# Optimization experiments

Hardware: AMD Instinct MI355X
Metric: run time of the kernel (lower is better)

The kernel has to match this reference:

```python
import jax, jax.numpy as jnp
import numpy as np

B, T, DIM = 2, 2048, 1024
H, HKV, D = 16, 4, 64
ROPE_DIMS = 32
ROPE_BASE = 10000.0


def fake_quant(w, n_bits):
    # per-output-row absmax symmetric fake quantization with STE
    half = 2 ** (n_bits - 1)
    w_max = jnp.maximum(jnp.max(jnp.abs(w), axis=1, keepdims=True), 1e-5)
    w_int = jnp.clip(jnp.round(w / w_max * half), -half, half - 1)
    w_q = w_int / half * w_max
    return w + jax.lax.stop_gradient(w_q - w)


def rms_norm(x):
    eps = jnp.finfo(x.dtype).eps
    return x * jax.lax.rsqrt(jnp.mean(x * x, axis=-1, keepdims=True) + eps)


def rope_tables(seq_len, dtype):
    inv_freq = 1.0 / (ROPE_BASE ** (jnp.arange(0, ROPE_DIMS, 2, dtype=jnp.float32) / ROPE_DIMS))
    t = jnp.arange(seq_len, dtype=jnp.float32)
    freqs = t[:, None] * inv_freq[None, :]  # [T, rope_dims/2]
    return jnp.cos(freqs).astype(dtype)[None, None], jnp.sin(freqs).astype(dtype)[None, None]


def apply_rotary(x, cos, sin):
    # partial rotary: rotate first ROPE_DIMS dims, pass the rest through
    x_rope, x_pass = x[..., :ROPE_DIMS], x[..., ROPE_DIMS:]
    half = ROPE_DIMS // 2
    x1, x2 = x_rope[..., :half], x_rope[..., half:]
    rot = jnp.concatenate([x1 * cos + x2 * sin, -x1 * sin + x2 * cos], axis=-1)
    return jnp.concatenate([rot, x_pass], axis=-1)


def setup_inputs() -> dict:
    key = jax.random.key(0)
    ks = jax.random.split(key, 5)
    kv_dim = HKV * D
    return {
        "x": jax.random.normal(ks[0], (B, T, DIM), dtype=jnp.float32),
        "w_q": jax.random.normal(ks[1], (DIM, DIM), dtype=jnp.float32) * 0.02,
        "w_k": jax.random.normal(ks[2], (kv_dim, DIM), dtype=jnp.float32) * 0.02,
        "w_v": jax.random.normal(ks[3], (kv_dim, DIM), dtype=jnp.float32) * 0.02,
        "w_proj": jax.random.normal(ks[4], (DIM, DIM), dtype=jnp.float32) * 0.02,
        "q_gain": jnp.full((H,), 1.5, dtype=jnp.float32),
    }


def reference(x, w_q, w_k, w_v, w_proj, q_gain):
    bsz, seqlen, dim = x.shape
    group = H // HKV

    # quantized (STE) projections
    q = x @ fake_quant(w_q, 6).T        # [B, T, DIM]
    k = x @ fake_quant(w_k, 6).T        # [B, T, HKV*D]
    v = x @ fake_quant(w_v, 5).T        # [B, T, HKV*D]

    q = q.reshape(bsz, seqlen, H, D).transpose(0, 2, 1, 3)    # [B, H, T, D]
    k = k.reshape(bsz, seqlen, HKV, D).transpose(0, 2, 1, 3)  # [B, HKV, T, D]
    v = v.reshape(bsz, seqlen, HKV, D).transpose(0, 2, 1, 3)  # [B, HKV, T, D]

    q = rms_norm(q)
    k = rms_norm(k)

    cos, sin = rope_tables(seqlen, q.dtype)
    q = apply_rotary(q, cos, sin)
    k = apply_rotary(k, cos, sin)

    q = q * q_gain.astype(q.dtype)[None, :, None, None]

    # grouped-query causal attention; scores kept in grouped [B,HKV,g,T,T] layout
    qg = q.reshape(bsz, HKV, group, seqlen, D)
    scores = jnp.einsum('bhgqd,bhkd->bhgqk', qg, k) / jnp.sqrt(jnp.asarray(D, q.dtype))
    causal = jnp.tril(jnp.ones((seqlen, seqlen), dtype=bool))
    scores = jnp.where(causal[None, None, None], scores, jnp.asarray(-jnp.inf, scores.dtype))
    att = jax.nn.softmax(scores, axis=-1)
    y = jnp.einsum('bhgqk,bhkd->bhgqd', att, v)               # [B, HKV, g, T, D]

    # xsa: orthogonalize y against normalized v (per kv head group)
    y_g = y.transpose(0, 3, 1, 2, 4)                           # [B, T, HKV, g, D]
    v_t = v.transpose(0, 2, 1, 3)                              # [B, T, HKV, D]
    vn = v_t / jnp.maximum(jnp.linalg.norm(v_t, axis=-1, keepdims=True), 1e-12)
    vn = vn[..., None, :]                                      # [B, T, HKV, 1, D]
    proj = jnp.sum(y_g * vn, axis=-1, keepdims=True) * vn
    y_out = (y_g - proj).reshape(bsz, seqlen, dim)

    return y_out @ fake_quant(w_proj, 5).T
```

## Files before the change

### kernel.cpp

```cpp
#include <hip/hip_runtime.h>
#include <math.h>

typedef unsigned short u16;
typedef __attribute__((ext_vector_type(8))) short short8;
typedef __attribute__((ext_vector_type(4))) float float4v;
typedef __attribute__((ext_vector_type(4))) u16 ushort4v;

namespace {
constexpr int kT    = 2048;
constexpr int kDim  = 1024;
constexpr int kH    = 16;
constexpr int kHKV  = 4;
constexpr int kD    = 64;
constexpr int kTok  = 4096;
constexpr int kQKVN = 1536;
}

__device__ __forceinline__ u16 f2bf(float f) {
  unsigned int u = __builtin_bit_cast(unsigned int, f);
  u = (u + 0x7FFFu + ((u >> 16) & 1u)) >> 16;
  return (u16)u;
}

__global__ __launch_bounds__(256) void prep_kernel(
    const float* __restrict__ x,
    const float* __restrict__ w_q, const float* __restrict__ w_k,
    const float* __restrict__ w_v, const float* __restrict__ w_proj,
    u16* __restrict__ xb, u16* __restrict__ wqkv, u16* __restrict__ wpq,
    float2* __restrict__ ropetab)
{
  __shared__ float red[4];
  const int bid = blockIdx.x, tid = threadIdx.x;

  if (bid < 128) {
    const int idx = bid * 256 + tid;
    const int t = idx >> 4, i = idx & 15;
    const float fr = (float)t * powf(10000.0f, -(float)i * (1.0f / 16.0f));
    ropetab[idx] = make_float2(cosf(fr), sinf(fr));
    return;
  }
  if (bid < 2176) {
    const size_t i = ((size_t)(bid - 128) * 256 + tid) * 8;
    const float4 a = *(const float4*)(x + i);
    const float4 b = *(const float4*)(x + i + 4);
    short8 r;
    r[0] = (short)f2bf(a.x); r[1] = (short)f2bf(a.y);
    r[2] = (short)f2bf(a.z); r[3] = (short)f2bf(a.w);
    r[4] = (short)f2bf(b.x); r[5] = (short)f2bf(b.y);
    r[6] = (short)f2bf(b.z); r[7] = (short)f2bf(b.w);
    *(short8*)(xb + i) = r;
    return;
  }
  const int rid = bid - 2176;
  const float* src; u16* dst; float halfv;
  if (rid < 1024)      { src = w_q    + (size_t)rid * 1024;          dst = wqkv + (size_t)rid * 1024;          halfv = 32.0f; }
  else if (rid < 1280) { src = w_k    + (size_t)(rid - 1024) * 1024; dst = wqkv + (size_t)rid * 1024;          halfv = 32.0f; }
  else if (rid < 1536) { src = w_v    + (size_t)(rid - 1280) * 1024; dst = wqkv + (size_t)rid * 1024;          halfv = 16.0f; }
  else                 { src = w_proj + (size_t)(rid - 1536) * 1024; dst = wpq  + (size_t)(rid - 1536) * 1024; halfv = 16.0f; }

  const float4 v4 = *(const float4*)(src + tid * 4);
  float mx = fmaxf(fmaxf(fabsf(v4.x), fabsf(v4.y)), fmaxf(fabsf(v4.z), fabsf(v4.w)));
  #pragma unroll
  for (int m = 1; m < 64; m <<= 1) mx = fmaxf(mx, __shfl_xor(mx, m));
  if ((tid & 63) == 0) red[tid >> 6] = mx;
  __syncthreads();
  mx = fmaxf(fmaxf(red[0], red[1]), fmaxf(red[2], red[3]));
  const float wmax = fmaxf(mx, 1e-5f);
  const float inv_half = 1.0f / halfv;
  const float vals[4] = {v4.x, v4.y, v4.z, v4.w};
  ushort4v o;
  #pragma unroll
  for (int j = 0; j < 4; ++j) {
    float r = rintf(vals[j] / wmax * halfv);
    r = fminf(fmaxf(r, -halfv), halfv - 1.0f);
    o[j] = f2bf(r * inv_half * wmax);
  }
  *(ushort4v*)(dst + tid * 4) = o;
}

__global__ __launch_bounds__(256) void gemm128(
    const u16* __restrict__ A, const u16* __restrict__ W,
    float* __restrict__ C, int K, int ldc, u16* __restrict__ vTp)
{
  __shared__ u16 As[128][32];
  __shared__ u16 Ws[128][32];
  const int tid = threadIdx.x;
  const int lane = tid & 63, wv = tid >> 6;
  const int n = lane & 15, quad = lane >> 4;
  const int wm = (wv & 1) * 64, wn = (wv >> 1) * 64;
  const int m0 = blockIdx.y * 128, n0 = blockIdx.x * 128;
  const int sr = tid >> 2, sc = (tid & 3) * 8;
  const int scs = sc ^ ((sr & 3) * 8);

  float4v acc[4][4];
  #pragma unroll
  for (int mi = 0; mi < 4; ++mi)
    #pragma unroll
    for (int ni = 0; ni < 4; ++ni) { acc[mi][ni][0]=0.f; acc[mi][ni][1]=0.f; acc[mi][ni][2]=0.f; acc[mi][ni][3]=0.f; }

  for (int k0 = 0; k0 < K; k0 += 32) {
    const short8 a0 = *(const short8*)(A + (size_t)(m0 + sr) * K + k0 + sc);
    const short8 a1 = *(const short8*)(A + (size_t)(m0 + sr + 64) * K + k0 + sc);
    const short8 w0 = *(const short8*)(W + (size_t)(n0 + sr) * K + k0 + sc);
    const short8 w1 = *(const short8*)(W + (size_t)(n0 + sr + 64) * K + k0 + sc);
    __syncthreads();
    *(short8*)&As[sr][scs] = a0;  *(short8*)&As[sr + 64][scs] = a1;
    *(short8*)&Ws[sr][scs] = w0;  *(short8*)&Ws[sr + 64][scs] = w1;
    __syncthreads();
    short8 af[4], bf[4];
    #pragma unroll
    for (int mi = 0; mi < 4; ++mi)
      af[mi] = *(const short8*)&As[wm + mi * 16 + n][(quad * 8) ^ ((n & 3) * 8)];
    #pragma unroll
    for (int ni = 0; ni < 4; ++ni)
      bf[ni] = *(const short8*)&Ws[wn + ni * 16 + n][(quad * 8) ^ ((n & 3) * 8)];
    #pragma unroll
    for (int mi = 0; mi < 4; ++mi)
      #pragma unroll
      for (int ni = 0; ni < 4; ++ni)
        acc[mi][ni] = __builtin_amdgcn_mfma_f32_16x16x32_bf16(af[mi], bf[ni], acc[mi][ni], 0, 0, 0);
  }

  #pragma unroll
  for (int mi = 0; mi < 4; ++mi) {
    const int r0 = m0 + wm + mi * 16 + quad * 4;
    #pragma unroll
    for (int ni = 0; ni < 4; ++ni) {
      const int col = n0 + wn + ni * 16 + n;
      #pragma unroll
      for (int i = 0; i < 4; ++i)
        C[(size_t)(r0 + i) * ldc + col] = acc[mi][ni][i];
      if (vTp != nullptr && col >= 1280) {
        const int vd = col - 1280;
        const int kvh = vd >> 6, d = vd & 63;
        const int bb = r0 >> 11, t0 = r0 & 2047;
        ushort4v pk;
        pk[0] = f2bf(acc[mi][ni][0]); pk[1] = f2bf(acc[mi][ni][1]);
        pk[2] = f2bf(acc[mi][ni][2]); pk[3] = f2bf(acc[mi][ni][3]);
        *(ushort4v*)(vTp + ((size_t)((bb * kHKV + kvh) * kD + d)) * kT + t0) = pk;
      }
    }
  }
}

__global__ __launch_bounds__(256) void normrope_kernel(
    const float* __restrict__ qkv, const float* __restrict__ q_gain,
    const float2* __restrict__ ropetab,
    u16* __restrict__ qh, u16* __restrict__ kh)
{
  const int lane = threadIdx.x & 63;
  const int w    = threadIdx.x >> 6;
  const int rid  = blockIdx.x * 4 + w;
  const int slot = rid % 20;
  const int tok  = rid / 20;
  const int t    = tok & (kT - 1);
  const int b    = tok >> 11;

  const float* src;
  u16* dst;
  if (slot < 16) {
    src = qkv + (size_t)tok * kQKVN + slot * kD;
    dst = qh + ((size_t)(b * kH + slot) * kT + t) * kD;
  } else {
    const int kvh = slot - 16;
    src = qkv + (size_t)tok * kQKVN + kDim + kvh * kD;
    dst = kh + ((size_t)(b * kHKV + kvh) * kT + t) * kD;
  }

  const float x = src[lane];
  float ss = x * x;
  #pragma unroll
  for (int m = 1; m < 64; m <<= 1) ss += __shfl_xor(ss, m);
  const float xn = x * (1.0f / sqrtf(ss * (1.0f / 64.0f) + 1.1920929e-7f));
  const float other = __shfl_xor(xn, 16);
  float xr = xn;
  if (lane < 32) {
    const float2 cs = ropetab[t * 16 + (lane & 15)];
    xr = xn * cs.x + ((lane < 16) ? other : -other) * cs.y;
  }
  if (slot < 16) xr *= q_gain[slot] * 0.125f;
  dst[lane] = f2bf(xr);
}

__global__ __launch_bounds__(256) void attn_mfma(
    const u16* __restrict__ qh, const u16* __restrict__ kh,
    const u16* __restrict__ vT, const float* __restrict__ qkv,
    u16* __restrict__ yo)
{
  __shared__ u16 ks[64][64];
  __shared__ u16 vs[64][64];
  __shared__ u16 ps[4][16][64];

  const int tid = threadIdx.x;
  const int lane = tid & 63, wq = tid >> 6;
  const int n = lane & 15, quad = lane >> 4;
  const int p = blockIdx.x;
  const int h = blockIdx.y, b = blockIdx.z;
  const int kv = h >> 2;
  const int tiles[2] = {p, 31 - p};
  const u16* kbase = kh + ((size_t)(b * kHKV + kv) * kT) * kD;
  const u16* vbase = vT + ((size_t)(b * kHKV + kv) * kD) * kT;

  short8 qa[2][2];
  {
    const u16* qb = qh + ((size_t)(b * kH + h) * kT) * kD;
    #pragma unroll
    for (int u = 0; u < 2; ++u) {
      const size_t row = (size_t)(tiles[u] * 64 + wq * 16 + n) * kD;
      qa[u][0] = *(const short8*)(qb + row + quad * 8);
      qa[u][1] = *(const short8*)(qb + row + 32 + quad * 8);
    }
  }

  const int sr = tid >> 3;
  const int sc = (tid & 7) * 8;
  const int scs = sc ^ ((sr & 7) * 8);

  float l_r[2] = {0.0f, 0.0f};
  float4v acc[2][4];
  #pragma unroll
  for (int u = 0; u < 2; ++u)
    #pragma unroll
    for (int g = 0; g < 4; ++g) { acc[u][g][0]=0.f; acc[u][g][1]=0.f; acc[u][g][2]=0.f; acc[u][g][3]=0.f; }

  short8 kr0, kr1, vr0, vr1;
  auto loadKV = [&](int kt) {
    kr0 = *(const short8*)(kbase + (size_t)(kt * 64 + sr) * kD + sc);
    kr1 = *(const short8*)(kbase + (size_t)(kt * 64 + sr + 32) * kD + sc);
    vr0 = *(const short8*)(vbase + (size_t)sr * kT + kt * 64 + sc);
    vr1 = *(const short8*)(vbase + (size_t)(sr + 32) * kT + kt * 64 + sc);
  };

  auto process = [&](int u, int kt) {
    float4v s[4];
    #pragma unroll
    for (int g = 0; g < 4; ++g) { s[g][0]=0.f; s[g][1]=0.f; s[g][2]=0.f; s[g][3]=0.f; }
    #pragma unroll
    for (int g = 0; g < 4; ++g) {
      const short8 kb0 = *(const short8*)&ks[g * 16 + n][(quad * 8) ^ ((n & 7) * 8)];
      s[g] = __builtin_amdgcn_mfma_f32_16x16x32_bf16(kb0, qa[u][0], s[g], 0, 0, 0);
      const short8 kb1 = *(const short8*)&ks[g * 16 + n][(32 + quad * 8) ^ ((n & 7) * 8)];
      s[g] = __builtin_amdgcn_mfma_f32_16x16x32_bf16(kb1, qa[u][1], s[g], 0, 0, 0);
    }
    if (kt == tiles[u]) {
      const int mloc = wq * 16 + n;
      #pragma unroll
      for (int g = 0; g < 4; ++g)
        #pragma unroll
        for (int i = 0; i < 4; ++i)
          if (g * 16 + quad * 4 + i > mloc) s[g][i] = -__builtin_inff();
    }
    float pf[4][4]; float rs = 0.0f;
    #pragma unroll
    for (int g = 0; g < 4; ++g)
      #pragma unroll
      for (int i = 0; i < 4; ++i) { pf[g][i] = __expf(s[g][i] - 12.0f); rs += pf[g][i]; }
    rs += __shfl_xor(rs, 16);
    rs += __shfl_xor(rs, 32);
    l_r[u] += rs;
    #pragma unroll
    for (int g = 0; g < 4; ++g) {
      ushort4v pk;
      pk[0] = f2bf(pf[g][0]); pk[1] = f2bf(pf[g][1]);
      pk[2] = f2bf(pf[g][2]); pk[3] = f2bf(pf[g][3]);
      *(ushort4v*)&ps[wq][n][(g * 16 + quad * 4) ^ ((n & 7) * 8)] = pk;
    }
    const short8 pb0 = *(const short8*)&ps[wq][n][(quad * 8) ^ ((n & 7) * 8)];
    const short8 pb1 = *(const short8*)&ps[wq][n][(32 + quad * 8) ^ ((n & 7) * 8)];
    #pragma unroll
    for (int g = 0; g < 4; ++g) {
      const short8 vb0 = *(const short8*)&vs[g * 16 + n][(quad * 8) ^ ((n & 7) * 8)];
      acc[u][g] = __builtin_amdgcn_mfma_f32_16x16x32_bf16(vb0, pb0, acc[u][g], 0, 0, 0);
      const short8 vb1 = *(const short8*)&vs[g * 16 + n][(32 + quad * 8) ^ ((n & 7) * 8)];
      acc[u][g] = __builtin_amdgcn_mfma_f32_16x16x32_bf16(vb1, pb1, acc[u][g], 0, 0, 0);
    }
  };

  const int kmax = tiles[1];
  loadKV(0);
  for (int kt = 0; kt <= kmax; ++kt) {
    __syncthreads();
    *(short8*)&ks[sr][scs]      = kr0;
    *(short8*)&ks[sr + 32][scs] = kr1;
    *(short8*)&vs[sr][scs]      = vr0;
    *(short8*)&vs[sr + 32][scs] = vr1;
    __syncthreads();
    if (kt < kmax) loadKV(kt + 1);
    process(1, kt);
    if (kt <= tiles[0]) process(0, kt);
  }

  #pragma unroll
  for (int u = 0; u < 2; ++u) {
    const int tok = b * kT + tiles[u] * 64 + wq * 16 + n;
    const float invl = 1.0f / l_r[u];
    float4 vv[4]; float nn = 0.0f, syr = 0.0f;
    #pragma unroll
    for (int g = 0; g < 4; ++g) {
      vv[g] = *(const float4*)(qkv + (size_t)tok * kQKVN + kDim + kHKV * kD + kv * kD + g * 16 + quad * 4);
      nn  += vv[g].x * vv[g].x + vv[g].y * vv[g].y + vv[g].z * vv[g].z + vv[g].w * vv[g].w;
      syr += acc[u][g][0] * vv[g].x + acc[u][g][1] * vv[g].y + acc[u][g][2] * vv[g].z + acc[u][g][3] * vv[g].w;
    }
    nn  += __shfl_xor(nn, 16);  nn  += __shfl_xor(nn, 32);
    syr += __shfl_xor(syr, 16); syr += __shfl_xor(syr, 32);
    const float inv = 1.0f / fmaxf(sqrtf(nn), 1e-12f);
    const float coef = syr * invl * inv * inv;
    #pragma unroll
    for (int g = 0; g < 4; ++g) {
      const float vf[4] = {vv[g].x, vv[g].y, vv[g].z, vv[g].w};
      ushort4v ow;
      #pragma unroll
      for (int i = 0; i < 4; ++i)
        ow[i] = f2bf(acc[u][g][i] * invl - coef * vf[i]);
      *(ushort4v*)(yo + (size_t)tok * kDim + h * kD + g * 16 + quad * 4) = ow;
    }
  }
}

extern "C" void kernel_launch(void* const* d_in, const int* in_sizes, int n_in,
                              void* d_out, int out_size, void* d_ws, size_t ws_size,
                              hipStream_t stream) {
  (void)in_sizes; (void)n_in; (void)out_size; (void)ws_size;
  const float* x      = (const float*)d_in[0];
  const float* w_q    = (const float*)d_in[1];
  const float* w_k    = (const float*)d_in[2];
  const float* w_v    = (const float*)d_in[3];
  const float* w_proj = (const float*)d_in[4];
  const float* q_gain = (const float*)d_in[5];

  char* wsb = (char*)d_ws;
  u16* wqkv = (u16*)wsb;  wsb += (size_t)1536 * 1024 * 2;
  u16* wpq  = (u16*)wsb;  wsb += (size_t)1024 * 1024 * 2;
  u16* xb   = (u16*)wsb;  wsb += (size_t)kTok * kDim * 2;
  float* qkv = (float*)wsb; wsb += (size_t)kTok * kQKVN * 4;
  u16* qh   = (u16*)wsb;  wsb += (size_t)kTok * kDim * 2;
  u16* khb  = (u16*)wsb;  wsb += (size_t)kTok * kHKV * kD * 2;
  u16* vTb  = (u16*)wsb;  wsb += (size_t)kTok * kHKV * kD * 2;
  u16* yo   = (u16*)wsb;  wsb += (size_t)kTok * kDim * 2;
  float2* ropetab = (float2*)wsb; wsb += (size_t)kT * 16 * sizeof(float2);

  prep_kernel<<<4736, 256, 0, stream>>>(x, w_q, w_k, w_v, w_proj,
                                        xb, wqkv, wpq, ropetab);

  gemm128<<<dim3(12, 32), 256, 0, stream>>>(xb, wqkv, qkv, kDim, kQKVN, vTb);

  normrope_kernel<<<kTok * 20 / 4, 256, 0, stream>>>(qkv, q_gain, ropetab, qh, khb);

  attn_mfma<<<dim3(16, kH, 2), 256, 0, stream>>>(qh, khb, vTb, qkv, yo);

  gemm128<<<dim3(8, 32), 256, 0, stream>>>(yo, wpq, (float*)d_out, kDim, kDim, nullptr);
}
```

Before: 198.2 us.

## Fuse RMS-norm and RoPE into QKV GEMM epilogue with 128x64 tiles

Removes the separate normrope kernel and the fp32 qkv intermediate. The QKV GEMM now uses 128x64 tiles so each block column matches one head, and its epilogue applies RMS norm, rotary and q_gain before writing bf16 q/k. V is written both transposed in bf16 and as a compact fp32 copy for the XSA step. The GEMM core also gains register prefetch of the next K slice, and both GEMMs launch more, smaller blocks, at the cost of less reuse per tile.

Result: faster. 167.4 us (-15.5%).

```diff
diff --git a/kernel.cpp b/kernel.cpp
--- a/kernel.cpp
+++ b/kernel.cpp
@@ -78,113 +78,129 @@
   *(ushort4v*)(dst + tid * 4) = o;
 }
 
-__global__ __launch_bounds__(256) void gemm128(
+#define GEMM_CORE(A_, W_, K_, NCOL0_)                                          \
+  __shared__ u16 As[128][32];                                                  \
+  __shared__ u16 Bs[64][32];                                                   \
+  const int tid = threadIdx.x;                                                 \
+  const int lane = tid & 63, wv = tid >> 6;                                    \
+  const int n = lane & 15, quad = lane >> 4;                                   \
+  const int wm = wv * 32;                                                      \
+  const int m0 = blockIdx.y * 128;                                             \
+  const int sr = tid >> 2, sc = (tid & 3) * 8;                                 \
+  const int scs = sc ^ ((sr & 3) * 8);                                         \
+  float4v acc[2][4];                                                           \
+  _Pragma("unroll")                                                            \
+  for (int mi = 0; mi < 2; ++mi)                                               \
+    _Pragma("unroll")                                                          \
+    for (int ni = 0; ni < 4; ++ni) {                                           \
+      acc[mi][ni][0]=0.f; acc[mi][ni][1]=0.f;                                  \
+      acc[mi][ni][2]=0.f; acc[mi][ni][3]=0.f; }                                \
+  short8 a0r, a1r, b0r;                                                        \
+  a0r = *(const short8*)(A_ + (size_t)(m0 + sr) * K_ + sc);                    \
+  a1r = *(const short8*)(A_ + (size_t)(m0 + sr + 64) * K_ + sc);               \
+  b0r = *(const short8*)(W_ + (size_t)(NCOL0_ + sr) * K_ + sc);                \
+  for (int k0 = 0; k0 < K_; k0 += 32) {                                        \
+    __syncthreads();                                                           \
+    *(short8*)&As[sr][scs] = a0r;  *(short8*)&As[sr + 64][scs] = a1r;          \
+    *(short8*)&Bs[sr][scs] = b0r;                                              \
+    __syncthreads();                                                           \
+    if (k0 + 32 < K_) {                                                        \
+      a0r = *(const short8*)(A_ + (size_t)(m0 + sr) * K_ + k0 + 32 + sc);      \
+      a1r = *(const short8*)(A_ + (size_t)(m0 + sr + 64) * K_ + k0 + 32 + sc); \
+      b0r = *(const short8*)(W_ + (size_t)(NCOL0_ + sr) * K_ + k0 + 32 + sc);  \
+    }                                                                          \
+    short8 af[2], bf[4];                                                       \
+    _Pragma("unroll")                                                          \
+    for (int mi = 0; mi < 2; ++mi)                                             \
+      af[mi] = *(const short8*)&As[wm + mi * 16 + n][(quad * 8) ^ ((n & 3) * 8)]; \
+    _Pragma("unroll")                                                          \
+    for (int ni = 0; ni < 4; ++ni)                                             \
+      bf[ni] = *(const short8*)&Bs[ni * 16 + n][(quad * 8) ^ ((n & 3) * 8)];   \
+    _Pragma("unroll")                                                          \
+    for (int mi = 0; mi < 2; ++mi)                                             \
+      _Pragma("unroll")                                                        \
+      for (int ni = 0; ni < 4; ++ni)                                           \
+        acc[mi][ni] = __builtin_amdgcn_mfma_f32_16x16x32_bf16(af[mi], bf[ni], acc[mi][ni], 0, 0, 0); \
+  }
+
+__global__ __launch_bounds__(256) void gemm_qkv(
     const u16* __restrict__ A, const u16* __restrict__ W,
-    float* __restrict__ C, int K, int ldc, u16* __restrict__ vTp)
+    const float2* __restrict__ ropetab, const float* __restrict__ q_gain,
+    u16* __restrict__ qh, u16* __restrict__ kh,
+    u16* __restrict__ vT, float* __restrict__ vcmp)
 {
-  __shared__ u16 As[128][32];
-  __shared__ u16 Ws[128][32];
-  const int tid = threadIdx.x;
-  const int lane = tid & 63, wv = tid >> 6;
-  const int n = lane & 15, quad = lane >> 4;
-  const int wm = (wv & 1) * 64, wn = (wv >> 1) * 64;
-  const int m0 = blockIdx.y * 128, n0 = blockIdx.x * 128;
-  const int sr = tid >> 2, sc = (tid & 3) * 8;
-  const int scs = sc ^ ((sr & 3) * 8);
-
-  float4v acc[4][4];
-  #pragma unroll
-  for (int mi = 0; mi < 4; ++mi)
-    #pragma unroll
-    for (int ni = 0; ni < 4; ++ni) { acc[mi][ni][0]=0.f; acc[mi][ni][1]=0.f; acc[mi][ni][2]=0.f; acc[mi][ni][3]=0.f; }
-
-  for (int k0 = 0; k0 < K; k0 += 32) {
-    const short8 a0 = *(const short8*)(A + (size_t)(m0 + sr) * K + k0 + sc);
-    const short8 a1 = *(const short8*)(A + (size_t)(m0 + sr + 64) * K + k0 + sc);
-    const short8 w0 = *(const short8*)(W + (size_t)(n0 + sr) * K + k0 + sc);
-    const short8 w1 = *(const short8*)(W + (size_t)(n0 + sr + 64) * K + k0 + sc);
-    __syncthreads();
-    *(short8*)&As[sr][scs] = a0;  *(short8*)&As[sr + 64][scs] = a1;
-    *(short8*)&Ws[sr][scs] = w0;  *(short8*)&Ws[sr + 64][scs] = w1;
-    __syncthreads();
-    short8 af[4], bf[4];
-    #pragma unroll
-    for (int mi = 0; mi < 4; ++mi)
-      af[mi] = *(const short8*)&As[wm + mi * 16 + n][(quad * 8) ^ ((n & 3) * 8)];
-    #pragma unroll
-    for (int ni = 0; ni < 4; ++ni)
-      bf[ni] = *(const short8*)&Ws[wn + ni * 16 + n][(quad * 8) ^ ((n & 3) * 8)];
-    #pragma unroll
-    for (int mi = 0; mi < 4; ++mi)
-      #pragma unroll
-      for (int ni = 0; ni < 4; ++ni)
-        acc[mi][ni] = __builtin_amdgcn_mfma_f32_16x16x32_bf16(af[mi], bf[ni], acc[mi][ni], 0, 0, 0);
-  }
-
-  #pragma unroll
-  for (int mi = 0; mi < 4; ++mi) {
-    const int r0 = m0 + wm + mi * 16 + quad * 4;
-    #pragma unroll
-    for (int ni = 0; ni < 4; ++ni) {
-      const int col = n0 + wn + ni * 16 + n;
-      #pragma unroll
-      for (int i = 0; i < 4; ++i)
-        C[(size_t)(r0 + i) * ldc + col] = acc[mi][ni][i];
-      if (vTp != nullptr && col >= 1280) {
-        const int vd = col - 1280;
-        const int kvh = vd >> 6, d = vd & 63;
-        const int bb = r0 >> 11, t0 = r0 & 2047;
+  GEMM_CORE(A, W, kDim, (int)(blockIdx.x * 64))
+
+  const int p = blockIdx.x;
+  const int rbase = m0 + wm;
+  const int bI = rbase >> 11;
+
+  if (p < 20) {
+    const float gain = (p < 16) ? q_gain[p] * 0.125f : 1.0f;
+    u16* dst = (p < 16) ? qh + ((size_t)(bI * kH + p) * kT) * kD
+                        : kh + ((size_t)(bI * kHKV + (p - 16)) * kT) * kD;
+    #pragma unroll
+    for (int mi = 0; mi < 2; ++mi)
+      #pragma unroll
+      for (int i = 0; i < 4; ++i) {
+        const int row = rbase + mi * 16 + quad * 4 + i;
+        const int t = row & (kT - 1);
+        float v[4];
+        #pragma unroll
+        for (int ni = 0; ni < 4; ++ni) v[ni] = acc[mi][ni][i];
+        float ss = v[0]*v[0] + v[1]*v[1] + v[2]*v[2] + v[3]*v[3];
+        #pragma unroll
+        for (int m = 1; m < 16; m <<= 1) ss += __shfl_xor(ss, m);
+        const float rr = 1.0f / sqrtf(ss * (1.0f / 64.0f) + 1.1920929e-7f);
+        #pragma unroll
+        for (int ni = 0; ni < 4; ++ni) v[ni] *= rr;
+        const float2 cs = ropetab[t * 16 + n];
+        const float r0 =  v[0] * cs.x + v[1] * cs.y;
+        const float r1 = -v[0] * cs.y + v[1] * cs.x;
+        v[0] = r0; v[1] = r1;
+        #pragma unroll
+        for (int ni = 0; ni < 4; ++ni)
+          dst[(size_t)t * kD + ni * 16 + n] = f2bf(v[ni] * gain);
+      }
+  } else {
+    const int kvh = p - 20;
+    u16* vTb = vT + ((size_t)(bI * kHKV + kvh) * kD) * kT;
+    #pragma unroll
+    for (int mi = 0; mi < 2; ++mi) {
+      const int t0 = (rbase + mi * 16 + quad * 4) & (kT - 1);
+      #pragma unroll
+      for (int ni = 0; ni < 4; ++ni) {
+        const int d = ni * 16 + n;
         ushort4v pk;
         pk[0] = f2bf(acc[mi][ni][0]); pk[1] = f2bf(acc[mi][ni][1]);
         pk[2] = f2bf(acc[mi][ni][2]); pk[3] = f2bf(acc[mi][ni][3]);
-        *(ushort4v*)(vTp + ((size_t)((bb * kHKV + kvh) * kD + d)) * kT + t0) = pk;
+        *(ushort4v*)(vTb + (size_t)d * kT + t0) = pk;
+        #pragma unroll
+        for (int i = 0; i < 4; ++i)
+          vcmp[(size_t)(rbase + mi * 16 + quad * 4 + i) * (kHKV * kD) + kvh * kD + d] = acc[mi][ni][i];
       }
     }
   }
 }
 
-__global__ __launch_bounds__(256) void normrope_kernel(
-    const float* __restrict__ qkv, const float* __restrict__ q_gain,
-    const float2* __restrict__ ropetab,
-    u16* __restrict__ qh, u16* __restrict__ kh)
+__global__ __launch_bounds__(256) void gemm_out(
+    const u16* __restrict__ A, const u16* __restrict__ W,
+    float* __restrict__ C)
 {
-  const int lane = threadIdx.x & 63;
-  const int w    = threadIdx.x >> 6;
-  const int rid  = blockIdx.x * 4 + w;
-  const int slot = rid % 20;
-  const int tok  = rid / 20;
-  const int t    = tok & (kT - 1);
-  const int b    = tok >> 11;
-
-  const float* src;
-  u16* dst;
-  if (slot < 16) {
-    src = qkv + (size_t)tok * kQKVN + slot * kD;
-    dst = qh + ((size_t)(b * kH + slot) * kT + t) * kD;
-  } else {
-    const int kvh = slot - 16;
-    src = qkv + (size_t)tok * kQKVN + kDim + kvh * kD;
-    dst = kh + ((size_t)(b * kHKV + kvh) * kT + t) * kD;
-  }
-
-  const float x = src[lane];
-  float ss = x * x;
-  #pragma unroll
-  for (int m = 1; m < 64; m <<= 1) ss += __shfl_xor(ss, m);
-  const float xn = x * (1.0f / sqrtf(ss * (1.0f / 64.0f) + 1.1920929e-7f));
-  const float other = __shfl_xor(xn, 16);
-  float xr = xn;
-  if (lane < 32) {
-    const float2 cs = ropetab[t * 16 + (lane & 15)];
-    xr = xn * cs.x + ((lane < 16) ? other : -other) * cs.y;
-  }
-  if (slot < 16) xr *= q_gain[slot] * 0.125f;
-  dst[lane] = f2bf(xr);
+  GEMM_CORE(A, W, kDim, (int)(blockIdx.x * 64))
+  const int n0 = blockIdx.x * 64;
+  #pragma unroll
+  for (int mi = 0; mi < 2; ++mi)
+    #pragma unroll
+    for (int ni = 0; ni < 4; ++ni)
+      #pragma unroll
+      for (int i = 0; i < 4; ++i)
+        C[(size_t)(m0 + wm + mi * 16 + quad * 4 + i) * kDim + n0 + ni * 16 + n] = acc[mi][ni][i];
 }
 
 __global__ __launch_bounds__(256) void attn_mfma(
     const u16* __restrict__ qh, const u16* __restrict__ kh,
-    const u16* __restrict__ vT, const float* __restrict__ qkv,
+    const u16* __restrict__ vT, const float* __restrict__ vcmp,
     u16* __restrict__ yo)
 {
   __shared__ u16 ks[64][64];
@@ -297,7 +313,7 @@
     float4 vv[4]; float nn = 0.0f, syr = 0.0f;
     #pragma unroll
     for (int g = 0; g < 4; ++g) {
-      vv[g] = *(const float4*)(qkv + (size_t)tok * kQKVN + kDim + kHKV * kD + kv * kD + g * 16 + quad * 4);
+      vv[g] = *(const float4*)(vcmp + (size_t)tok * (kHKV * kD) + kv * kD + g * 16 + quad * 4);
       nn  += vv[g].x * vv[g].x + vv[g].y * vv[g].y + vv[g].z * vv[g].z + vv[g].w * vv[g].w;
       syr += acc[u][g][0] * vv[g].x + acc[u][g][1] * vv[g].y + acc[u][g][2] * vv[g].z + acc[u][g][3] * vv[g].w;
     }
@@ -332,21 +348,20 @@
   u16* wqkv = (u16*)wsb;  wsb += (size_t)1536 * 1024 * 2;
   u16* wpq  = (u16*)wsb;  wsb += (size_t)1024 * 1024 * 2;
   u16* xb   = (u16*)wsb;  wsb += (size_t)kTok * kDim * 2;
-  float* qkv = (float*)wsb; wsb += (size_t)kTok * kQKVN * 4;
   u16* qh   = (u16*)wsb;  wsb += (size_t)kTok * kDim * 2;
   u16* khb  = (u16*)wsb;  wsb += (size_t)kTok * kHKV * kD * 2;
   u16* vTb  = (u16*)wsb;  wsb += (size_t)kTok * kHKV * kD * 2;
   u16* yo   = (u16*)wsb;  wsb += (size_t)kTok * kDim * 2;
+  float* vcmp = (float*)wsb; wsb += (size_t)kTok * kHKV * kD * 4;
   float2* ropetab = (float2*)wsb; wsb += (size_t)kT * 16 * sizeof(float2);
 
   prep_kernel<<<4736, 256, 0, stream>>>(x, w_q, w_k, w_v, w_proj,
                                         xb, wqkv, wpq, ropetab);
 
-  gemm128<<<dim3(12, 32), 256, 0, stream>>>(xb, wqkv, qkv, kDim, kQKVN, vTb);
-
-  normrope_kernel<<<kTok * 20 / 4, 256, 0, stream>>>(qkv, q_gain, ropetab, qh, khb);
-
-  attn_mfma<<<dim3(16, kH, 2), 256, 0, stream>>>(qh, khb, vTb, qkv, yo);
-
-  gemm128<<<dim3(8, 32), 256, 0, stream>>>(yo, wpq, (float*)d_out, kDim, kDim, nullptr);
-}
+  gemm_qkv<<<dim3(24, 32), 256, 0, stream>>>(xb, wqkv, ropetab, q_gain,
+                                             qh, khb, vTb, vcmp);
+
+  attn_mfma<<<dim3(16, kH, 2), 256, 0, stream>>>(qh, khb, vTb, vcmp, yo);
+
+  gemm_out<<<dim3(16, 32), 256, 0, stream>>>(yo, wpq, (float*)d_out);
+}
```
